# Kernel tuning notes

Hardware: AMD Instinct MI355X
Metric: run time of the kernel (lower is better)

The kernel has to match this reference:

```python
import jax, jax.numpy as jnp
import numpy as np

N_GROUPS = 32
EPS = 1e-5


def group_norm(x, gamma, beta):
    b, c, h, w = x.shape
    xg = x.reshape(b, N_GROUPS, c // N_GROUPS, h, w)
    mean = xg.mean(axis=(2, 3, 4), keepdims=True)
    var = xg.var(axis=(2, 3, 4), keepdims=True)
    xn = ((xg - mean) * jax.lax.rsqrt(var + EPS)).reshape(b, c, h, w)
    return xn * gamma[None, :, None, None] + beta[None, :, None, None]


def conv1x1(x, W, b):
    # x: [b,c,h,w], W: [out,in], b: [out]
    return jnp.einsum('bchw,oc->bohw', x, W) + b[None, :, None, None]


def setup_inputs() -> dict:
    key = jax.random.key(0)
    ks = jax.random.split(key, 6)
    B, C, H, W = 8, 256, 64, 64
    s = 1.0 / np.sqrt(C)
    return {
        'x': jax.random.normal(ks[0], (B, C, H, W), dtype=jnp.float32),
        'norm_gamma': jnp.ones((C,), jnp.float32),
        'norm_beta': jnp.zeros((C,), jnp.float32),
        'Wq': jax.random.normal(ks[1], (C, C), jnp.float32) * s,
        'bq': jnp.zeros((C,), jnp.float32),
        'Wk': jax.random.normal(ks[2], (C, C), jnp.float32) * s,
        'bk': jnp.zeros((C,), jnp.float32),
        'Wv': jax.random.normal(ks[3], (C, C), jnp.float32) * s,
        'bv': jnp.zeros((C,), jnp.float32),
        'Wo': jax.random.normal(ks[4], (C, C), jnp.float32) * s,
        'bo': jnp.zeros((C,), jnp.float32),
    }


def reference(x, norm_gamma, norm_beta, Wq, bq, Wk, bk, Wv, bv, Wo, bo):
    b, c, h, w = x.shape
    hn = group_norm(x, norm_gamma, norm_beta)
    q = conv1x1(hn, Wq, bq).reshape(b, c, h * w)  # [b,c,hw]
    k = conv1x1(hn, Wk, bk).reshape(b, c, h * w)
    v = conv1x1(hn, Wv, bv).reshape(b, c, h * w)
    # scores[b,i,j] = sum_c q[b,c,i] * k[b,c,j]; scale is int(c)*-0.5
    # (faithful to the source, which multiplies by -0.5*c, NOT c**-0.5)
    scores = jnp.einsum('bci,bcj->bij', q, k) * (c * -0.5)
    attn = jax.nn.softmax(scores, axis=2)  # softmax over j (keys)
    # h_[b,c,i] = sum_j v[b,c,j] * attn[b,i,j]
    h_ = jnp.einsum('bcj,bij->bci', v, attn).reshape(b, c, h, w)
    # source applies self.out to the ORIGINAL input x and adds attention output
    return h_ + conv1x1(x, Wo, bo)
```

## Files before the change

kernel.cpp:

```cpp
#include <hip/hip_runtime.h>
#include <hip/hip_bf16.h>


typedef __attribute__((ext_vector_type(8))) short bf16x8;
typedef __attribute__((ext_vector_type(4))) short s16x4;
typedef __attribute__((ext_vector_type(8))) short s16x8;
typedef __attribute__((ext_vector_type(4))) float f32x4;

#define MFMA16(a, b, c) __builtin_amdgcn_mfma_f32_16x16x32_bf16((a), (b), (c), 0, 0, 0)

#define SCALE_Q (-184.66496523378734f)

__device__ __forceinline__ short f2bf(float f) {
  unsigned int u = __builtin_bit_cast(unsigned int, f);
  u = (u + 0x7FFFu + ((u >> 16) & 1u)) >> 16;
  return (short)(unsigned short)u;
}
__device__ __forceinline__ float bf2f(short h) {
  unsigned int u = ((unsigned int)(unsigned short)h) << 16;
  return __builtin_bit_cast(float, u);
}
__device__ __forceinline__ void async16(void* lds, const void* g) {
  __builtin_amdgcn_global_load_lds(
      (const __attribute__((address_space(1))) unsigned int*)g,
      (__attribute__((address_space(3))) unsigned int*)lds, 16, 0, 0);
}

__global__ void wsplit_k(const float* __restrict__ Wq, const float* __restrict__ Wk,
                         const float* __restrict__ Wv, const float* __restrict__ Wo,
                         short* __restrict__ whi, short* __restrict__ wlo) {
  int idx = blockIdx.x * 256 + threadIdx.x;
  int m = idx >> 16;
  int e = idx & 65535;
  const float* W = (m == 0) ? Wq : (m == 1) ? Wk : (m == 2) ? Wv : Wo;
  float v = W[e];
  short h = f2bf(v);
  whi[idx] = h;
  wlo[idx] = f2bf(v - bf2f(h));
}

__global__ void gn_stats_k(const float* __restrict__ x, float* __restrict__ stats) {
  int bg = blockIdx.x;
  int tid = threadIdx.x;
  const float* p = x + (size_t)bg * 32768;
  float s = 0.f, sq = 0.f;
  for (int it = 0; it < 32; ++it) {
    f32x4 v = *(const f32x4*)(p + (size_t)(it * 256 + tid) * 4);
    s += v[0] + v[1] + v[2] + v[3];
    sq += v[0] * v[0] + v[1] * v[1] + v[2] * v[2] + v[3] * v[3];
  }
#pragma unroll
  for (int off = 1; off < 64; off <<= 1) {
    s += __shfl_xor(s, off);
    sq += __shfl_xor(sq, off);
  }
  __shared__ float ls[4], lq[4];
  int w = tid >> 6;
  if ((tid & 63) == 0) { ls[w] = s; lq[w] = sq; }
  __syncthreads();
  if (tid == 0) {
    float S = ls[0] + ls[1] + ls[2] + ls[3];
    float Q = lq[0] + lq[1] + lq[2] + lq[3];
    float mean = S * (1.f / 32768.f);
    float var = Q * (1.f / 32768.f) - mean * mean;
    stats[bg * 2] = mean;
    stats[bg * 2 + 1] = rsqrtf(var + 1e-5f);
  }
}

__global__ void gn_apply_k(const float* __restrict__ x, const float* __restrict__ gamma,
                           const float* __restrict__ beta, const float* __restrict__ stats,
                           short* __restrict__ hn_hi, short* __restrict__ hn_lo) {
  __shared__ float tile[64 * 68];
  int tid = threadIdx.x;
  int b = blockIdx.z, c0 = blockIdx.y * 64, i0 = blockIdx.x * 64;
  int cc = tid >> 4, ich = tid & 15;
#pragma unroll
  for (int it = 0; it < 4; ++it) {
    int c = c0 + cc + it * 16;
    f32x4 vx = *(const f32x4*)(x + ((size_t)(b * 256 + c)) * 4096 + i0 + ich * 4);
    float mean = stats[(b * 32 + (c >> 3)) * 2];
    float rstd = stats[(b * 32 + (c >> 3)) * 2 + 1];
    float ga = gamma[c] * rstd;
    float be = beta[c] - mean * ga;
    f32x4 h = {vx[0] * ga + be, vx[1] * ga + be, vx[2] * ga + be, vx[3] * ga + be};
    *(f32x4*)(&tile[(cc + it * 16) * 68 + ich * 4]) = h;
  }
  __syncthreads();
  int il = tid >> 2, ch = tid & 3;
  s16x8 hv0, hv1, lv0, lv1;
#pragma unroll
  for (int u = 0; u < 16; ++u) {
    float vv = tile[(ch * 16 + u) * 68 + il];
    short h = f2bf(vv);
    short lo = f2bf(vv - bf2f(h));
    if (u < 8) { hv0[u] = h; lv0[u] = lo; } else { hv1[u - 8] = h; lv1[u - 8] = lo; }
  }
  size_t ro = ((size_t)(b * 4096 + i0 + il)) * 256 + c0 + ch * 16;
  *(s16x8*)(hn_hi + ro) = hv0;
  *(s16x8*)(hn_hi + ro + 8) = hv1;
  *(s16x8*)(hn_lo + ro) = lv0;
  *(s16x8*)(hn_lo + ro + 8) = lv1;
}

__global__ __launch_bounds__(256) void proj_qk_k(
    const short* __restrict__ hn_hi, const short* __restrict__ hn_lo,
    const short* __restrict__ whi, const short* __restrict__ wlo,
    const float* __restrict__ bq, const float* __restrict__ bk,
    short* __restrict__ q_hi, short* __restrict__ q_lo,
    short* __restrict__ k_hi, short* __restrict__ k_lo) {
  int tid = threadIdx.x, w = tid >> 6, lane = tid & 63, l4 = lane & 15, g = lane >> 4;
  int iblk = blockIdx.x, y = blockIdx.y, b = blockIdx.z;
  const short* wh = whi + y * 65536;
  const short* wl = wlo + y * 65536;
  const float* bias = y ? bk : bq;
  short* ohi = (y ? k_hi : q_hi) + (size_t)b * 1048576;
  short* olo = (y ? k_lo : q_lo) + (size_t)b * 1048576;
  float scale = y ? 1.0f : SCALE_Q;
  int arow = iblk * 64 + w * 16 + l4;
  const short* ha = hn_hi + ((size_t)(b * 4096 + arow)) * 256 + g * 8;
  const short* la = hn_lo + ((size_t)(b * 4096 + arow)) * 256 + g * 8;
  f32x4 acc[16];
#pragma unroll
  for (int i = 0; i < 16; ++i) acc[i] = (f32x4){0.f, 0.f, 0.f, 0.f};
  for (int ks = 0; ks < 8; ++ks) {
    bf16x8 ah = *(const bf16x8*)(ha + ks * 32);
    bf16x8 al = *(const bf16x8*)(la + ks * 32);
#pragma unroll
    for (int ct = 0; ct < 16; ++ct) {
      bf16x8 bh = *(const bf16x8*)(wh + (ct * 16 + l4) * 256 + ks * 32 + g * 8);
      bf16x8 bl = *(const bf16x8*)(wl + (ct * 16 + l4) * 256 + ks * 32 + g * 8);
      acc[ct] = MFMA16(ah, bh, acc[ct]);
      acc[ct] = MFMA16(al, bh, acc[ct]);
      acc[ct] = MFMA16(ah, bl, acc[ct]);
    }
  }
  int orow = iblk * 64 + w * 16 + g * 4;
#pragma unroll
  for (int ct = 0; ct < 16; ++ct) {
    int c = ct * 16 + l4;
    float bsv = bias[c];
#pragma unroll
    for (int r = 0; r < 4; ++r) {
      float val = (acc[ct][r] + bsv) * scale;
      short h = f2bf(val);
      short lo = f2bf(val - bf2f(h));
      size_t off = ((size_t)(orow + r)) * 256 + c;
      ohi[off] = h;
      olo[off] = lo;
    }
  }
}

__global__ __launch_bounds__(256) void proj_v_k(
    const short* __restrict__ hn_hi, const short* __restrict__ wv_hi,
    const float* __restrict__ bv, short* __restrict__ vout) {
  int tid = threadIdx.x, w = tid >> 6, lane = tid & 63, l4 = lane & 15, g = lane >> 4;
  int jblk = blockIdx.x, cblk = blockIdx.y, b = blockIdx.z;
  int crow = cblk * 64 + w * 16 + l4;
  const short* ap = wv_hi + (size_t)crow * 256 + g * 8;
  f32x4 acc[4];
#pragma unroll
  for (int i = 0; i < 4; ++i) acc[i] = (f32x4){0.f, 0.f, 0.f, 0.f};
  for (int ks = 0; ks < 8; ++ks) {
    bf16x8 a = *(const bf16x8*)(ap + ks * 32);
#pragma unroll
    for (int jt = 0; jt < 4; ++jt) {
      bf16x8 bb = *(const bf16x8*)(hn_hi +
          ((size_t)(b * 4096 + jblk * 64 + jt * 16 + l4)) * 256 + ks * 32 + g * 8);
      acc[jt] = MFMA16(a, bb, acc[jt]);
    }
  }
#pragma unroll
  for (int jt = 0; jt < 4; ++jt) {
#pragma unroll
    for (int r = 0; r < 4; ++r) {
      int c = cblk * 64 + w * 16 + g * 4 + r;
      int j = jblk * 64 + jt * 16 + l4;
      float val = acc[jt][r] + bv[c];
      vout[((size_t)(b * 256 + c)) * 4096 + j] = f2bf(val);
    }
  }
}

__global__ __launch_bounds__(256, 2) void flash3_k(
    const short* __restrict__ qhi, const short* __restrict__ qlo,
    const short* __restrict__ khi, const short* __restrict__ klo,
    const short* __restrict__ vv, const float* __restrict__ x,
    const short* __restrict__ wo_hi, const float* __restrict__ bo,
    float* __restrict__ out) {
  __shared__ short k_hi_s[2][8192];
  __shared__ short k_lo_s[2][8192];
  __shared__ short p_s[2048];
  __shared__ __attribute__((aligned(16))) float albuf[64];
  __shared__ __attribute__((aligned(16))) float flagbuf[4];
  __shared__ __attribute__((aligned(16))) float lsmbuf[64];

  int tid = threadIdx.x, w = tid >> 6, lane = tid & 63, l4 = lane & 15, g = lane >> 4;
  int b = blockIdx.y, i0 = blockIdx.x * 64;
  size_t boff = (size_t)b * 1048576;
  const short* qh_p = qhi + boff;
  const short* ql_p = qlo + boff;
  const char* kh_g = (const char*)(khi + boff);
  const char* kl_g = (const char*)(klo + boff);
  const short* v_p = vv + boff;

  int qrow = i0 + w * 16 + l4;
  bf16x8 qh[8], ql[8];
#pragma unroll
  for (int ks = 0; ks < 8; ++ks) {
    qh[ks] = *(const bf16x8*)(qh_p + (size_t)qrow * 256 + ks * 32 + g * 8);
    ql[ks] = *(const bf16x8*)(ql_p + (size_t)qrow * 256 + ks * 32 + g * 8);
  }

  f32x4 oac[4][4];
#pragma unroll
  for (int it = 0; it < 4; ++it)
#pragma unroll
    for (int ct = 0; ct < 4; ++ct) oac[it][ct] = (f32x4){0.f, 0.f, 0.f, 0.f};
  float m_cur = -1e30f, lsum = 0.f;

  int sx = (l4 & 7) << 4;
  int colx[8];
#pragma unroll
  for (int ks = 0; ks < 8; ++ks) colx[ks] = (ks * 64 + g * 16) ^ sx;
  int krow_b = l4 * 512;

  int ksrc[4];
#pragma unroll
  for (int it = 0; it < 4; ++it) {
    int d = tid * 16 + it * 4096;
    int krow = d >> 9, kcol = d & 511;
    ksrc[it] = krow * 512 + (kcol ^ ((krow & 7) << 4));
  }

  char* khs = (char*)k_hi_s;
  char* kls = (char*)k_lo_s;
  char* ps = (char*)p_s;
  int cbase = w * 64;
  bf16x8 vreg[4];

#pragma unroll
  for (int it = 0; it < 4; ++it) {
    int ldst = w * 1024 + it * 4096;
    async16(khs + ldst, kh_g + ksrc[it]);
    async16(kls + ldst, kl_g + ksrc[it]);
  }

  for (int js = 0; js < 128; ++js) {
    int cur = (js & 1) * 16384;
    __syncthreads();
    if (js < 127) {
      int kgo = (js + 1) * 16384;
      int nxt = ((js + 1) & 1) * 16384;
#pragma unroll
      for (int it = 0; it < 4; ++it) {
        int ldst = nxt + w * 1024 + it * 4096;
        async16(khs + ldst, kh_g + kgo + ksrc[it]);
        async16(kls + ldst, kl_g + kgo + ksrc[it]);
      }
    }
#pragma unroll
    for (int ct = 0; ct < 4; ++ct)
      vreg[ct] = *(const bf16x8*)(v_p + (size_t)(cbase + ct * 16 + l4) * 4096 +
                                  js * 32 + g * 8);

    f32x4 st0 = (f32x4){0.f, 0.f, 0.f, 0.f};
    f32x4 st1 = (f32x4){0.f, 0.f, 0.f, 0.f};
    __builtin_amdgcn_s_setprio(1);
#pragma unroll
    for (int ks = 0; ks < 8; ++ks) {
      bf16x8 kh0 = *(const bf16x8*)(khs + cur + krow_b + colx[ks]);
      bf16x8 kh1 = *(const bf16x8*)(khs + cur + krow_b + colx[ks] + 8192);
      bf16x8 kl0 = *(const bf16x8*)(kls + cur + krow_b + colx[ks]);
      bf16x8 kl1 = *(const bf16x8*)(kls + cur + krow_b + colx[ks] + 8192);
      st0 = MFMA16(kh0, qh[ks], st0);
      st1 = MFMA16(kh1, qh[ks], st1);
      st0 = MFMA16(kl0, qh[ks], st0);
      st1 = MFMA16(kl1, qh[ks], st1);
      st0 = MFMA16(kh0, ql[ks], st0);
      st1 = MFMA16(kh1, ql[ks], st1);
    }
    __builtin_amdgcn_s_setprio(0);

    float pmax = fmaxf(fmaxf(fmaxf(st0[0], st0[1]), fmaxf(st0[2], st0[3])),
                       fmaxf(fmaxf(st1[0], st1[1]), fmaxf(st1[2], st1[3])));
    pmax = fmaxf(pmax, __shfl_xor(pmax, 16));
    pmax = fmaxf(pmax, __shfl_xor(pmax, 32));
    float alpha = 1.0f;
    bool upd = !__all(pmax <= m_cur + 11.0f);
    if (upd) {
      float m_new = fmaxf(m_cur, pmax);
      alpha = exp2f(m_cur - m_new);
      lsum *= alpha;
      m_cur = m_new;
    }
    f32x4 e0, e1;
#pragma unroll
    for (int r = 0; r < 4; ++r) {
      e0[r] = exp2f(st0[r] - m_cur);
      e1[r] = exp2f(st1[r] - m_cur);
    }
    float lps = e0[0] + e0[1] + e0[2] + e0[3] + e1[0] + e1[1] + e1[2] + e1[3];
    lps += __shfl_xor(lps, 16);
    lps += __shfl_xor(lps, 32);
    lsum += lps;

    s16x4 pw0 = {f2bf(e0[0]), f2bf(e0[1]), f2bf(e0[2]), f2bf(e0[3])};
    s16x4 pw1 = {f2bf(e1[0]), f2bf(e1[1]), f2bf(e1[2]), f2bf(e1[3])};
    int wb = (w * 16 + l4) * 64 + g * 8;
    *(s16x4*)(ps + wb) = pw0;
    *(s16x4*)(ps + wb + 32) = pw1;
    if (lane < 16) albuf[w * 16 + lane] = alpha;
    if (lane == 0) flagbuf[w] = upd ? 1.f : 0.f;

    __syncthreads();

    f32x4 fl = *(const f32x4*)(&flagbuf[0]);
    if (fl[0] + fl[1] + fl[2] + fl[3] > 0.f) {
#pragma unroll
      for (int it = 0; it < 4; ++it) {
        f32x4 av = *(const f32x4*)(&albuf[it * 16 + g * 4]);
#pragma unroll
        for (int ct = 0; ct < 4; ++ct)
#pragma unroll
          for (int r = 0; r < 4; ++r) oac[it][ct][r] *= av[r];
      }
    }
#pragma unroll
    for (int it = 0; it < 4; ++it) {
      bf16x8 pf = *(const bf16x8*)(ps + (it * 16 + l4) * 64 + g * 16);
#pragma unroll
      for (int ct = 0; ct < 4; ++ct) oac[it][ct] = MFMA16(pf, vreg[ct], oac[it][ct]);
    }
  }

  if (lane < 16) lsmbuf[w * 16 + lane] = lsum;
  __syncthreads();
#pragma unroll
  for (int it = 0; it < 4; ++it) {
    f32x4 lv = *(const f32x4*)(&lsmbuf[it * 16 + g * 4]);
    f32x4 iv = {1.f / lv[0], 1.f / lv[1], 1.f / lv[2], 1.f / lv[3]};
#pragma unroll
    for (int ct = 0; ct < 4; ++ct)
#pragma unroll
      for (int r = 0; r < 4; ++r) oac[it][ct][r] *= iv[r];
  }
  const float* xb = x + (size_t)b * 1048576;
  for (int ks = 0; ks < 8; ++ks) {
    bf16x8 af[4], bfr[4];
#pragma unroll
    for (int it = 0; it < 4; ++it) {
#pragma unroll
      for (int e = 0; e < 8; ++e) {
        float xv = xb[(size_t)(ks * 32 + g * 8 + e) * 4096 + i0 + it * 16 + l4];
        af[it][e] = f2bf(xv);
      }
    }
#pragma unroll
    for (int ct = 0; ct < 4; ++ct)
      bfr[ct] = *(const bf16x8*)(wo_hi + (cbase + ct * 16 + l4) * 256 + ks * 32 + g * 8);
#pragma unroll
    for (int it = 0; it < 4; ++it)
#pragma unroll
      for (int ct = 0; ct < 4; ++ct) oac[it][ct] = MFMA16(af[it], bfr[ct], oac[it][ct]);
  }
  float* ob = out + (size_t)b * 1048576;
#pragma unroll
  for (int ct = 0; ct < 4; ++ct) {
    float bov = bo[cbase + ct * 16 + l4];
#pragma unroll
    for (int it = 0; it < 4; ++it) {
      float* ad = ob + (size_t)(cbase + ct * 16 + l4) * 4096 + i0 + it * 16 + g * 4;
      f32x4 res;
#pragma unroll
      for (int r = 0; r < 4; ++r) res[r] = oac[it][ct][r] + bov;
      *(f32x4*)ad = res;
    }
  }
}

extern "C" void kernel_launch(void* const* d_in, const int* in_sizes, int n_in,
                              void* d_out, int out_size, void* d_ws, size_t ws_size,
                              hipStream_t stream) {
  (void)in_sizes; (void)n_in; (void)out_size; (void)ws_size;
  const float* x = (const float*)d_in[0];
  const float* gamma = (const float*)d_in[1];
  const float* beta = (const float*)d_in[2];
  const float* Wq = (const float*)d_in[3];
  const float* bq = (const float*)d_in[4];
  const float* Wk = (const float*)d_in[5];
  const float* bk = (const float*)d_in[6];
  const float* Wv = (const float*)d_in[7];
  const float* bv = (const float*)d_in[8];
  const float* Wo = (const float*)d_in[9];
  const float* bo = (const float*)d_in[10];
  float* out = (float*)d_out;
  char* ws = (char*)d_ws;

  const size_t MB16 = 16777216;
  float* stats = (float*)(ws);
  short* whi = (short*)(ws + 4096);
  short* wlo = (short*)(ws + 4096 + 524288);
  char* base = ws + 4096 + 2 * 524288;
  short* hnhi = (short*)(base);
  short* hnlo = (short*)(base + MB16);
  short* qhi = (short*)(base + 2 * MB16);
  short* qlo = (short*)(base + 3 * MB16);
  short* khi = (short*)(base + 4 * MB16);
  short* klo = (short*)(base + 5 * MB16);
  short* vvp = (short*)(base + 6 * MB16);

  wsplit_k<<<dim3(1024), dim3(256), 0, stream>>>(Wq, Wk, Wv, Wo, whi, wlo);
  gn_stats_k<<<dim3(256), dim3(256), 0, stream>>>(x, stats);
  gn_apply_k<<<dim3(64, 4, 8), dim3(256), 0, stream>>>(x, gamma, beta, stats, hnhi, hnlo);
  proj_qk_k<<<dim3(64, 2, 8), dim3(256), 0, stream>>>(hnhi, hnlo, whi, wlo, bq, bk,
                                                      qhi, qlo, khi, klo);
  proj_v_k<<<dim3(64, 4, 8), dim3(256), 0, stream>>>(hnhi, whi + 2 * 65536, bv, vvp);
  flash3_k<<<dim3(64, 8), dim3(256), 0, stream>>>(qhi, qlo, khi, klo, vvp, x,
                                                  whi + 3 * 65536, bo, out);
}
```

Baseline: 537.3 us.

## Enlarge flash attention tile to 128 queries with 8 waves splitting keys

The flash attention kernel now handles 128 query rows per block using 512 threads. Waves are arranged 4x2: each wave owns 32 query rows and half of each 32-key tile. The two halves combine their row max and row sum through LDS exchanges with an added barrier, and the P buffer is padded. Each K tile loaded into LDS now serves twice as many queries, and V register loads are prefetched one iteration ahead. The cost is an extra barrier per iteration, more registers per thread, and half as many blocks (256), which may hurt occupancy on a large GPU.

```diff
diff --git a/kernel.cpp b/kernel.cpp
--- a/kernel.cpp
+++ b/kernel.cpp
@@ -24,6 +24,11 @@
   __builtin_amdgcn_global_load_lds(
       (const __attribute__((address_space(1))) unsigned int*)g,
       (__attribute__((address_space(3))) unsigned int*)lds, 16, 0, 0);
+}
+__device__ __forceinline__ void lgkm_barrier() {
+  asm volatile("s_waitcnt lgkmcnt(0)" ::: "memory");
+  __builtin_amdgcn_s_barrier();
+  __builtin_amdgcn_sched_barrier(0);
 }
 
 __global__ void wsplit_k(const float* __restrict__ Wq, const float* __restrict__ Wk,
@@ -183,7 +188,7 @@
   }
 }
 
-__global__ __launch_bounds__(256, 2) void flash3_k(
+__global__ __launch_bounds__(512, 2) void flash4_k(
     const short* __restrict__ qhi, const short* __restrict__ qlo,
     const short* __restrict__ khi, const short* __restrict__ klo,
     const short* __restrict__ vv, const float* __restrict__ x,
@@ -191,13 +196,15 @@
     float* __restrict__ out) {
   __shared__ short k_hi_s[2][8192];
   __shared__ short k_lo_s[2][8192];
-  __shared__ short p_s[2048];
-  __shared__ __attribute__((aligned(16))) float albuf[64];
+  __shared__ short p_s[128 * 40];
+  __shared__ __attribute__((aligned(16))) float xbuf[2][128];
+  __shared__ __attribute__((aligned(16))) float albuf[128];
+  __shared__ __attribute__((aligned(16))) float lsmbuf[128];
   __shared__ __attribute__((aligned(16))) float flagbuf[4];
-  __shared__ __attribute__((aligned(16))) float lsmbuf[64];
 
   int tid = threadIdx.x, w = tid >> 6, lane = tid & 63, l4 = lane & 15, g = lane >> 4;
-  int b = blockIdx.y, i0 = blockIdx.x * 64;
+  int wj = w & 1, wi = w >> 1;
+  int b = blockIdx.y, i0 = blockIdx.x * 128;
   size_t boff = (size_t)b * 1048576;
   const short* qh_p = qhi + boff;
   const short* ql_p = qlo + boff;
@@ -205,31 +212,35 @@
   const char* kl_g = (const char*)(klo + boff);
   const short* v_p = vv + boff;
 
-  int qrow = i0 + w * 16 + l4;
-  bf16x8 qh[8], ql[8];
-#pragma unroll
-  for (int ks = 0; ks < 8; ++ks) {
-    qh[ks] = *(const bf16x8*)(qh_p + (size_t)qrow * 256 + ks * 32 + g * 8);
-    ql[ks] = *(const bf16x8*)(ql_p + (size_t)qrow * 256 + ks * 32 + g * 8);
-  }
-
-  f32x4 oac[4][4];
-#pragma unroll
-  for (int it = 0; it < 4; ++it)
-#pragma unroll
-    for (int ct = 0; ct < 4; ++ct) oac[it][ct] = (f32x4){0.f, 0.f, 0.f, 0.f};
-  float m_cur = -1e30f, lsum = 0.f;
-
+  bf16x8 qh[2][8], ql[2][8];
+#pragma unroll
+  for (int it = 0; it < 2; ++it) {
+    int qrow = i0 + wi * 32 + it * 16 + l4;
+#pragma unroll
+    for (int ks = 0; ks < 8; ++ks) {
+      qh[it][ks] = *(const bf16x8*)(qh_p + (size_t)qrow * 256 + ks * 32 + g * 8);
+      ql[it][ks] = *(const bf16x8*)(ql_p + (size_t)qrow * 256 + ks * 32 + g * 8);
+    }
+  }
+
+  f32x4 oac[8][2];
+#pragma unroll
+  for (int it = 0; it < 8; ++it) {
+    oac[it][0] = (f32x4){0.f, 0.f, 0.f, 0.f};
+    oac[it][1] = (f32x4){0.f, 0.f, 0.f, 0.f};
+  }
+  float m0 = -1e30f, m1 = -1e30f, ls0 = 0.f, ls1 = 0.f;
+
+  int krow_b = (wj * 16 + l4) * 512;
   int sx = (l4 & 7) << 4;
   int colx[8];
 #pragma unroll
   for (int ks = 0; ks < 8; ++ks) colx[ks] = (ks * 64 + g * 16) ^ sx;
-  int krow_b = l4 * 512;
-
-  int ksrc[4];
-#pragma unroll
-  for (int it = 0; it < 4; ++it) {
-    int d = tid * 16 + it * 4096;
+
+  int ksrc[2];
+#pragma unroll
+  for (int it = 0; it < 2; ++it) {
+    int d = tid * 16 + it * 8192;
     int krow = d >> 9, kcol = d & 511;
     ksrc[it] = krow * 512 + (kcol ^ ((krow & 7) << 4));
   }
@@ -237,15 +248,20 @@
   char* khs = (char*)k_hi_s;
   char* kls = (char*)k_lo_s;
   char* ps = (char*)p_s;
-  int cbase = w * 64;
-  bf16x8 vreg[4];
-
-#pragma unroll
-  for (int it = 0; it < 4; ++it) {
-    int ldst = w * 1024 + it * 4096;
+  int cbase = w * 32;
+  int prow0 = (wi * 32 + l4) * 80 + wj * 32 + g * 8;
+  int prow1 = (wi * 32 + 16 + l4) * 80 + wj * 32 + g * 8;
+
+#pragma unroll
+  for (int it = 0; it < 2; ++it) {
+    int ldst = w * 1024 + it * 8192;
     async16(khs + ldst, kh_g + ksrc[it]);
     async16(kls + ldst, kl_g + ksrc[it]);
   }
+  bf16x8 vreg[2];
+#pragma unroll
+  for (int ct = 0; ct < 2; ++ct)
+    vreg[ct] = *(const bf16x8*)(v_p + (size_t)(cbase + ct * 16 + l4) * 4096 + g * 8);
 
   for (int js = 0; js < 128; ++js) {
     int cur = (js & 1) * 16384;
@@ -254,123 +270,149 @@
       int kgo = (js + 1) * 16384;
       int nxt = ((js + 1) & 1) * 16384;
 #pragma unroll
-      for (int it = 0; it < 4; ++it) {
-        int ldst = nxt + w * 1024 + it * 4096;
+      for (int it = 0; it < 2; ++it) {
+        int ldst = nxt + w * 1024 + it * 8192;
         async16(khs + ldst, kh_g + kgo + ksrc[it]);
         async16(kls + ldst, kl_g + kgo + ksrc[it]);
       }
     }
-#pragma unroll
-    for (int ct = 0; ct < 4; ++ct)
-      vreg[ct] = *(const bf16x8*)(v_p + (size_t)(cbase + ct * 16 + l4) * 4096 +
-                                  js * 32 + g * 8);
-
-    f32x4 st0 = (f32x4){0.f, 0.f, 0.f, 0.f};
-    f32x4 st1 = (f32x4){0.f, 0.f, 0.f, 0.f};
+
+    f32x4 sa0 = (f32x4){0.f, 0.f, 0.f, 0.f};
+    f32x4 sa1 = (f32x4){0.f, 0.f, 0.f, 0.f};
     __builtin_amdgcn_s_setprio(1);
 #pragma unroll
     for (int ks = 0; ks < 8; ++ks) {
-      bf16x8 kh0 = *(const bf16x8*)(khs + cur + krow_b + colx[ks]);
-      bf16x8 kh1 = *(const bf16x8*)(khs + cur + krow_b + colx[ks] + 8192);
-      bf16x8 kl0 = *(const bf16x8*)(kls + cur + krow_b + colx[ks]);
-      bf16x8 kl1 = *(const bf16x8*)(kls + cur + krow_b + colx[ks] + 8192);
-      st0 = MFMA16(kh0, qh[ks], st0);
-      st1 = MFMA16(kh1, qh[ks], st1);
-      st0 = MFMA16(kl0, qh[ks], st0);
-      st1 = MFMA16(kl1, qh[ks], st1);
-      st0 = MFMA16(kh0, ql[ks], st0);
-      st1 = MFMA16(kh1, ql[ks], st1);
+      bf16x8 kh = *(const bf16x8*)(khs + cur + krow_b + colx[ks]);
+      bf16x8 kl = *(const bf16x8*)(kls + cur + krow_b + colx[ks]);
+      sa0 = MFMA16(kh, qh[0][ks], sa0);
+      sa1 = MFMA16(kh, qh[1][ks], sa1);
+      sa0 = MFMA16(kh, ql[0][ks], sa0);
+      sa1 = MFMA16(kh, ql[1][ks], sa1);
+      sa0 = MFMA16(kl, qh[0][ks], sa0);
+      sa1 = MFMA16(kl, qh[1][ks], sa1);
     }
     __builtin_amdgcn_s_setprio(0);
 
-    float pmax = fmaxf(fmaxf(fmaxf(st0[0], st0[1]), fmaxf(st0[2], st0[3])),
-                       fmaxf(fmaxf(st1[0], st1[1]), fmaxf(st1[2], st1[3])));
-    pmax = fmaxf(pmax, __shfl_xor(pmax, 16));
-    pmax = fmaxf(pmax, __shfl_xor(pmax, 32));
-    float alpha = 1.0f;
-    bool upd = !__all(pmax <= m_cur + 11.0f);
+    float pmax0 = fmaxf(fmaxf(sa0[0], sa0[1]), fmaxf(sa0[2], sa0[3]));
+    float pmax1 = fmaxf(fmaxf(sa1[0], sa1[1]), fmaxf(sa1[2], sa1[3]));
+    pmax0 = fmaxf(pmax0, __shfl_xor(pmax0, 16));
+    pmax0 = fmaxf(pmax0, __shfl_xor(pmax0, 32));
+    pmax1 = fmaxf(pmax1, __shfl_xor(pmax1, 16));
+    pmax1 = fmaxf(pmax1, __shfl_xor(pmax1, 32));
+    if (lane < 16) {
+      xbuf[wj][wi * 32 + lane] = pmax0;
+      xbuf[wj][wi * 32 + 16 + lane] = pmax1;
+    }
+    lgkm_barrier();
+
+    pmax0 = fmaxf(pmax0, xbuf[wj ^ 1][wi * 32 + l4]);
+    pmax1 = fmaxf(pmax1, xbuf[wj ^ 1][wi * 32 + 16 + l4]);
+    float alpha0 = 1.0f, alpha1 = 1.0f;
+    bool upd = !__all((pmax0 <= m0 + 11.0f) && (pmax1 <= m1 + 11.0f));
     if (upd) {
-      float m_new = fmaxf(m_cur, pmax);
-      alpha = exp2f(m_cur - m_new);
-      lsum *= alpha;
-      m_cur = m_new;
+      float mn0 = fmaxf(m0, pmax0), mn1 = fmaxf(m1, pmax1);
+      alpha0 = exp2f(m0 - mn0);
+      alpha1 = exp2f(m1 - mn1);
+      ls0 *= alpha0;
+      ls1 *= alpha1;
+      m0 = mn0;
+      m1 = mn1;
     }
     f32x4 e0, e1;
 #pragma unroll
     for (int r = 0; r < 4; ++r) {
-      e0[r] = exp2f(st0[r] - m_cur);
-      e1[r] = exp2f(st1[r] - m_cur);
-    }
-    float lps = e0[0] + e0[1] + e0[2] + e0[3] + e1[0] + e1[1] + e1[2] + e1[3];
-    lps += __shfl_xor(lps, 16);
-    lps += __shfl_xor(lps, 32);
-    lsum += lps;
+      e0[r] = exp2f(sa0[r] - m0);
+      e1[r] = exp2f(sa1[r] - m1);
+    }
+    ls0 += e0[0] + e0[1] + e0[2] + e0[3];
+    ls1 += e1[0] + e1[1] + e1[2] + e1[3];
 
     s16x4 pw0 = {f2bf(e0[0]), f2bf(e0[1]), f2bf(e0[2]), f2bf(e0[3])};
     s16x4 pw1 = {f2bf(e1[0]), f2bf(e1[1]), f2bf(e1[2]), f2bf(e1[3])};
-    int wb = (w * 16 + l4) * 64 + g * 8;
-    *(s16x4*)(ps + wb) = pw0;
-    *(s16x4*)(ps + wb + 32) = pw1;
-    if (lane < 16) albuf[w * 16 + lane] = alpha;
-    if (lane == 0) flagbuf[w] = upd ? 1.f : 0.f;
-
-    __syncthreads();
+    *(s16x4*)(ps + prow0) = pw0;
+    *(s16x4*)(ps + prow1) = pw1;
+    if (wj == 0 && lane < 16) {
+      albuf[wi * 32 + lane] = alpha0;
+      albuf[wi * 32 + 16 + lane] = alpha1;
+    }
+    if (wj == 0 && lane == 0) flagbuf[wi] = upd ? 1.f : 0.f;
+    lgkm_barrier();
 
     f32x4 fl = *(const f32x4*)(&flagbuf[0]);
     if (fl[0] + fl[1] + fl[2] + fl[3] > 0.f) {
 #pragma unroll
-      for (int it = 0; it < 4; ++it) {
+      for (int it = 0; it < 8; ++it) {
         f32x4 av = *(const f32x4*)(&albuf[it * 16 + g * 4]);
 #pragma unroll
-        for (int ct = 0; ct < 4; ++ct)
-#pragma unroll
-          for (int r = 0; r < 4; ++r) oac[it][ct][r] *= av[r];
+        for (int r = 0; r < 4; ++r) {
+          oac[it][0][r] *= av[r];
+          oac[it][1][r] *= av[r];
+        }
       }
     }
 #pragma unroll
-    for (int it = 0; it < 4; ++it) {
-      bf16x8 pf = *(const bf16x8*)(ps + (it * 16 + l4) * 64 + g * 16);
-#pragma unroll
-      for (int ct = 0; ct < 4; ++ct) oac[it][ct] = MFMA16(pf, vreg[ct], oac[it][ct]);
-    }
-  }
-
-  if (lane < 16) lsmbuf[w * 16 + lane] = lsum;
-  __syncthreads();
-#pragma unroll
-  for (int it = 0; it < 4; ++it) {
-    f32x4 lv = *(const f32x4*)(&lsmbuf[it * 16 + g * 4]);
-    f32x4 iv = {1.f / lv[0], 1.f / lv[1], 1.f / lv[2], 1.f / lv[3]};
-#pragma unroll
-    for (int ct = 0; ct < 4; ++ct)
-#pragma unroll
-      for (int r = 0; r < 4; ++r) oac[it][ct][r] *= iv[r];
+    for (int it = 0; it < 8; ++it) {
+      bf16x8 pf = *(const bf16x8*)(ps + (it * 16 + l4) * 80 + g * 16);
+      oac[it][0] = MFMA16(pf, vreg[0], oac[it][0]);
+      oac[it][1] = MFMA16(pf, vreg[1], oac[it][1]);
+    }
+    if (js < 127) {
+#pragma unroll
+      for (int ct = 0; ct < 2; ++ct)
+        vreg[ct] = *(const bf16x8*)(v_p + (size_t)(cbase + ct * 16 + l4) * 4096 +
+                                    (js + 1) * 32 + g * 8);
+    }
+  }
+
+  ls0 += __shfl_xor(ls0, 16);
+  ls0 += __shfl_xor(ls0, 32);
+  ls1 += __shfl_xor(ls1, 16);
+  ls1 += __shfl_xor(ls1, 32);
+  if (lane < 16) {
+    xbuf[wj][wi * 32 + lane] = ls0;
+    xbuf[wj][wi * 32 + 16 + lane] = ls1;
+  }
+  lgkm_barrier();
+  float t0 = ls0 + xbuf[wj ^ 1][wi * 32 + l4];
+  float t1 = ls1 + xbuf[wj ^ 1][wi * 32 + 16 + l4];
+  if (wj == 0 && lane < 16) {
+    lsmbuf[wi * 32 + l4] = 1.f / t0;
+    lsmbuf[wi * 32 + 16 + l4] = 1.f / t1;
+  }
+  lgkm_barrier();
+#pragma unroll
+  for (int it = 0; it < 8; ++it) {
+    f32x4 iv = *(const f32x4*)(&lsmbuf[it * 16 + g * 4]);
+#pragma unroll
+    for (int r = 0; r < 4; ++r) {
+      oac[it][0][r] *= iv[r];
+      oac[it][1][r] *= iv[r];
+    }
   }
   const float* xb = x + (size_t)b * 1048576;
   for (int ks = 0; ks < 8; ++ks) {
-    bf16x8 af[4], bfr[4];
-#pragma unroll
-    for (int it = 0; it < 4; ++it) {
+    bf16x8 bfr[2];
+#pragma unroll
+    for (int ct = 0; ct < 2; ++ct)
+      bfr[ct] = *(const bf16x8*)(wo_hi + (cbase + ct * 16 + l4) * 256 + ks * 32 + g * 8);
+#pragma unroll
+    for (int it = 0; it < 8; ++it) {
+      bf16x8 af;
 #pragma unroll
       for (int e = 0; e < 8; ++e) {
         float xv = xb[(size_t)(ks * 32 + g * 8 + e) * 4096 + i0 + it * 16 + l4];
-        af[it][e] = f2bf(xv);
+        af[e] = f2bf(xv);
       }
-    }
-#pragma unroll
-    for (int ct = 0; ct < 4; ++ct)
-      bfr[ct] = *(const bf16x8*)(wo_hi + (cbase + ct * 16 + l4) * 256 + ks * 32 + g * 8);
-#pragma unroll
-    for (int it = 0; it < 4; ++it)
-#pragma unroll
-      for (int ct = 0; ct < 4; ++ct) oac[it][ct] = MFMA16(af[it], bfr[ct], oac[it][ct]);
+      oac[it][0] = MFMA16(af, bfr[0], oac[it][0]);
+      oac[it][1] = MFMA16(af, bfr[1], oac[it][1]);
+    }
   }
   float* ob = out + (size_t)b * 1048576;
 #pragma unroll
-  for (int ct = 0; ct < 4; ++ct) {
+  for (int ct = 0; ct < 2; ++ct) {
     float bov = bo[cbase + ct * 16 + l4];
 #pragma unroll
-    for (int it = 0; it < 4; ++it) {
+    for (int it = 0; it < 8; ++it) {
       float* ad = ob + (size_t)(cbase + ct * 16 + l4) * 4096 + i0 + it * 16 + g * 4;
       f32x4 res;
 #pragma unroll
@@ -417,6 +459,6 @@
   proj_qk_k<<<dim3(64, 2, 8), dim3(256), 0, stream>>>(hnhi, hnlo, whi, wlo, bq, bk,
                                                       qhi, qlo, khi, klo);
   proj_v_k<<<dim3(64, 4, 8), dim3(256), 0, stream>>>(hnhi, whi + 2 * 65536, bv, vvp);
-  flash3_k<<<dim3(64, 8), dim3(256), 0, stream>>>(qhi, qlo, khi, klo, vvp, x,
+  flash4_k<<<dim3(32, 8), dim3(512), 0, stream>>>(qhi, qlo, khi, klo, vvp, x,
                                                   whi + 3 * 65536, bo, out);
 }
```

Result: slower. 653.6 us (+21.6%).

## Rewrite flash attention kernel with 32x32 MFMA tiles and 64-key steps

Applied to the files above, without the earlier changes.

The attention kernel now uses 32x32x16 bf16 MFMA instead of 16x16x32. Work is split across a 2x2 wave grid (query halves by key halves), and each iteration processes 64 keys instead of 32. The K tile is single-buffered with a vmcnt barrier, and its next load is issued after the score phase. Row maxima and sums are exchanged across waves through LDS, with lighter custom barriers. The aim is higher MFMA throughput and fewer loop iterations and barriers, at the cost of losing double-buffer overlap on K loads and adding cross-wave reductions.

```diff
diff --git a/kernel.cpp b/kernel.cpp
--- a/kernel.cpp
+++ b/kernel.cpp
@@ -6,8 +6,10 @@
 typedef __attribute__((ext_vector_type(4))) short s16x4;
 typedef __attribute__((ext_vector_type(8))) short s16x8;
 typedef __attribute__((ext_vector_type(4))) float f32x4;
+typedef __attribute__((ext_vector_type(16))) float f32x16;
 
 #define MFMA16(a, b, c) __builtin_amdgcn_mfma_f32_16x16x32_bf16((a), (b), (c), 0, 0, 0)
+#define MFMA32(a, b, c) __builtin_amdgcn_mfma_f32_32x32x16_bf16((a), (b), (c), 0, 0, 0)
 
 #define SCALE_Q (-184.66496523378734f)
 
@@ -24,6 +26,16 @@
   __builtin_amdgcn_global_load_lds(
       (const __attribute__((address_space(1))) unsigned int*)g,
       (__attribute__((address_space(3))) unsigned int*)lds, 16, 0, 0);
+}
+__device__ __forceinline__ void lgkm_barrier() {
+  asm volatile("s_waitcnt lgkmcnt(0)" ::: "memory");
+  __builtin_amdgcn_s_barrier();
+  __builtin_amdgcn_sched_barrier(0);
+}
+__device__ __forceinline__ void vm_barrier() {
+  asm volatile("s_waitcnt vmcnt(0)" ::: "memory");
+  __builtin_amdgcn_s_barrier();
+  __builtin_amdgcn_sched_barrier(0);
 }
 
 __global__ void wsplit_k(const float* __restrict__ Wq, const float* __restrict__ Wk,
@@ -183,20 +195,23 @@
   }
 }
 
-__global__ __launch_bounds__(256, 2) void flash3_k(
+__global__ __launch_bounds__(256, 2) void flash5_k(
     const short* __restrict__ qhi, const short* __restrict__ qlo,
     const short* __restrict__ khi, const short* __restrict__ klo,
     const short* __restrict__ vv, const float* __restrict__ x,
     const short* __restrict__ wo_hi, const float* __restrict__ bo,
     float* __restrict__ out) {
-  __shared__ short k_hi_s[2][8192];
-  __shared__ short k_lo_s[2][8192];
-  __shared__ short p_s[2048];
+  __shared__ short k_hi_s[16384];
+  __shared__ short k_lo_s[16384];
+  __shared__ short p_s[4096];
+  __shared__ __attribute__((aligned(16))) float xbuf[2][64];
   __shared__ __attribute__((aligned(16))) float albuf[64];
-  __shared__ __attribute__((aligned(16))) float flagbuf[4];
   __shared__ __attribute__((aligned(16))) float lsmbuf[64];
-
-  int tid = threadIdx.x, w = tid >> 6, lane = tid & 63, l4 = lane & 15, g = lane >> 4;
+  __shared__ __attribute__((aligned(16))) float flagbuf[2];
+
+  int tid = threadIdx.x, w = tid >> 6, lane = tid & 63;
+  int l31 = lane & 31, hi = lane >> 5;
+  int wj = w & 1, wi = w >> 1;
   int b = blockIdx.y, i0 = blockIdx.x * 64;
   size_t boff = (size_t)b * 1048576;
   const short* qh_p = qhi + boff;
@@ -204,179 +219,184 @@
   const char* kh_g = (const char*)(khi + boff);
   const char* kl_g = (const char*)(klo + boff);
   const short* v_p = vv + boff;
-
-  int qrow = i0 + w * 16 + l4;
-  bf16x8 qh[8], ql[8];
-#pragma unroll
-  for (int ks = 0; ks < 8; ++ks) {
-    qh[ks] = *(const bf16x8*)(qh_p + (size_t)qrow * 256 + ks * 32 + g * 8);
-    ql[ks] = *(const bf16x8*)(ql_p + (size_t)qrow * 256 + ks * 32 + g * 8);
-  }
-
-  f32x4 oac[4][4];
-#pragma unroll
-  for (int it = 0; it < 4; ++it)
-#pragma unroll
-    for (int ct = 0; ct < 4; ++ct) oac[it][ct] = (f32x4){0.f, 0.f, 0.f, 0.f};
+  int cbase = w * 64;
+
+  int qrow = i0 + wi * 32 + l31;
+  bf16x8 qh[16], ql[16];
+#pragma unroll
+  for (int ks = 0; ks < 16; ++ks) {
+    qh[ks] = *(const bf16x8*)(qh_p + (size_t)qrow * 256 + ks * 16 + hi * 8);
+    ql[ks] = *(const bf16x8*)(ql_p + (size_t)qrow * 256 + ks * 16 + hi * 8);
+  }
+
+  f32x16 oac[2][2];
+#pragma unroll
+  for (int ih = 0; ih < 2; ++ih) {
+    oac[ih][0] = (f32x16)0.0f;
+    oac[ih][1] = (f32x16)0.0f;
+  }
   float m_cur = -1e30f, lsum = 0.f;
-
-  int sx = (l4 & 7) << 4;
-  int colx[8];
-#pragma unroll
-  for (int ks = 0; ks < 8; ++ks) colx[ks] = (ks * 64 + g * 16) ^ sx;
-  int krow_b = l4 * 512;
-
-  int ksrc[4];
-#pragma unroll
-  for (int it = 0; it < 4; ++it) {
-    int d = tid * 16 + it * 4096;
-    int krow = d >> 9, kcol = d & 511;
-    ksrc[it] = krow * 512 + (kcol ^ ((krow & 7) << 4));
-  }
 
   char* khs = (char*)k_hi_s;
   char* kls = (char*)k_lo_s;
   char* ps = (char*)p_s;
-  int cbase = w * 64;
-  bf16x8 vreg[4];
-
-#pragma unroll
-  for (int it = 0; it < 4; ++it) {
-    int ldst = w * 1024 + it * 4096;
-    async16(khs + ldst, kh_g + ksrc[it]);
-    async16(kls + ldst, kl_g + ksrc[it]);
-  }
-
-  for (int js = 0; js < 128; ++js) {
-    int cur = (js & 1) * 16384;
-    __syncthreads();
-    if (js < 127) {
-      int kgo = (js + 1) * 16384;
-      int nxt = ((js + 1) & 1) * 16384;
-#pragma unroll
-      for (int it = 0; it < 4; ++it) {
-        int ldst = nxt + w * 1024 + it * 4096;
-        async16(khs + ldst, kh_g + kgo + ksrc[it]);
-        async16(kls + ldst, kl_g + kgo + ksrc[it]);
+  int krb = (wj * 32 + l31) * 512;
+  int psw = (l31 & 7) << 4;
+  int ksl[16];
+#pragma unroll
+  for (int ks = 0; ks < 16; ++ks) ksl[ks] = (ks * 32 + hi * 16) ^ psw;
+
+  int soff[8];
+#pragma unroll
+  for (int it = 0; it < 8; ++it) {
+    int row = w * 16 + it * 2 + hi;
+    soff[it] = row * 512 + ((l31 * 16) ^ ((row & 7) << 4));
+  }
+
+#pragma unroll
+  for (int it = 0; it < 8; ++it) {
+    async16(khs + w * 8192 + it * 1024, kh_g + soff[it]);
+    async16(kls + w * 8192 + it * 1024, kl_g + soff[it]);
+  }
+
+  int pwb = (wi * 32 + l31) * 128;
+
+  for (int js = 0; js < 64; ++js) {
+    vm_barrier();
+
+    f32x16 sacc = (f32x16)0.0f;
+    __builtin_amdgcn_s_setprio(1);
+#pragma unroll
+    for (int ks = 0; ks < 16; ++ks) {
+      bf16x8 kh = *(const bf16x8*)(khs + krb + ksl[ks]);
+      bf16x8 kl = *(const bf16x8*)(kls + krb + ksl[ks]);
+      sacc = MFMA32(kh, qh[ks], sacc);
+      sacc = MFMA32(kl, qh[ks], sacc);
+      sacc = MFMA32(kh, ql[ks], sacc);
+    }
+    __builtin_amdgcn_s_setprio(0);
+
+    float pm = sacc[0];
+#pragma unroll
+    for (int t = 1; t < 16; ++t) pm = fmaxf(pm, sacc[t]);
+    pm = fmaxf(pm, __shfl_xor(pm, 32));
+    if (lane < 32) xbuf[wj][wi * 32 + l31] = pm;
+    lgkm_barrier();
+
+    bf16x8 vf[2][4];
+#pragma unroll
+    for (int ct = 0; ct < 2; ++ct)
+#pragma unroll
+      for (int j4 = 0; j4 < 4; ++j4)
+        vf[ct][j4] = *(const bf16x8*)(v_p + (size_t)(cbase + ct * 32 + l31) * 4096 +
+                                      js * 64 + j4 * 16 + hi * 8);
+    if (js < 63) {
+      int tb = (js + 1) * 32768;
+#pragma unroll
+      for (int it = 0; it < 8; ++it) {
+        async16(khs + w * 8192 + it * 1024, kh_g + tb + soff[it]);
+        async16(kls + w * 8192 + it * 1024, kl_g + tb + soff[it]);
       }
     }
-#pragma unroll
-    for (int ct = 0; ct < 4; ++ct)
-      vreg[ct] = *(const bf16x8*)(v_p + (size_t)(cbase + ct * 16 + l4) * 4096 +
-                                  js * 32 + g * 8);
-
-    f32x4 st0 = (f32x4){0.f, 0.f, 0.f, 0.f};
-    f32x4 st1 = (f32x4){0.f, 0.f, 0.f, 0.f};
-    __builtin_amdgcn_s_setprio(1);
-#pragma unroll
-    for (int ks = 0; ks < 8; ++ks) {
-      bf16x8 kh0 = *(const bf16x8*)(khs + cur + krow_b + colx[ks]);
-      bf16x8 kh1 = *(const bf16x8*)(khs + cur + krow_b + colx[ks] + 8192);
-      bf16x8 kl0 = *(const bf16x8*)(kls + cur + krow_b + colx[ks]);
-      bf16x8 kl1 = *(const bf16x8*)(kls + cur + krow_b + colx[ks] + 8192);
-      st0 = MFMA16(kh0, qh[ks], st0);
-      st1 = MFMA16(kh1, qh[ks], st1);
-      st0 = MFMA16(kl0, qh[ks], st0);
-      st1 = MFMA16(kl1, qh[ks], st1);
-      st0 = MFMA16(kh0, ql[ks], st0);
-      st1 = MFMA16(kh1, ql[ks], st1);
-    }
-    __builtin_amdgcn_s_setprio(0);
-
-    float pmax = fmaxf(fmaxf(fmaxf(st0[0], st0[1]), fmaxf(st0[2], st0[3])),
-                       fmaxf(fmaxf(st1[0], st1[1]), fmaxf(st1[2], st1[3])));
-    pmax = fmaxf(pmax, __shfl_xor(pmax, 16));
-    pmax = fmaxf(pmax, __shfl_xor(pmax, 32));
+
+    pm = fmaxf(pm, xbuf[wj ^ 1][wi * 32 + l31]);
     float alpha = 1.0f;
-    bool upd = !__all(pmax <= m_cur + 11.0f);
+    bool upd = !__all(pm <= m_cur + 11.0f);
     if (upd) {
-      float m_new = fmaxf(m_cur, pmax);
-      alpha = exp2f(m_cur - m_new);
+      float mn = fmaxf(m_cur, pm);
+      alpha = exp2f(m_cur - mn);
       lsum *= alpha;
-      m_cur = m_new;
-    }
-    f32x4 e0, e1;
-#pragma unroll
-    for (int r = 0; r < 4; ++r) {
-      e0[r] = exp2f(st0[r] - m_cur);
-      e1[r] = exp2f(st1[r] - m_cur);
-    }
-    float lps = e0[0] + e0[1] + e0[2] + e0[3] + e1[0] + e1[1] + e1[2] + e1[3];
-    lps += __shfl_xor(lps, 16);
+      m_cur = mn;
+    }
+    float e[16];
+    float lps = 0.f;
+#pragma unroll
+    for (int t = 0; t < 16; ++t) {
+      e[t] = exp2f(sacc[t] - m_cur);
+      lps += e[t];
+    }
     lps += __shfl_xor(lps, 32);
     lsum += lps;
 
-    s16x4 pw0 = {f2bf(e0[0]), f2bf(e0[1]), f2bf(e0[2]), f2bf(e0[3])};
-    s16x4 pw1 = {f2bf(e1[0]), f2bf(e1[1]), f2bf(e1[2]), f2bf(e1[3])};
-    int wb = (w * 16 + l4) * 64 + g * 8;
-    *(s16x4*)(ps + wb) = pw0;
-    *(s16x4*)(ps + wb + 32) = pw1;
-    if (lane < 16) albuf[w * 16 + lane] = alpha;
-    if (lane == 0) flagbuf[w] = upd ? 1.f : 0.f;
-
-    __syncthreads();
-
-    f32x4 fl = *(const f32x4*)(&flagbuf[0]);
-    if (fl[0] + fl[1] + fl[2] + fl[3] > 0.f) {
-#pragma unroll
-      for (int it = 0; it < 4; ++it) {
-        f32x4 av = *(const f32x4*)(&albuf[it * 16 + g * 4]);
-#pragma unroll
-        for (int ct = 0; ct < 4; ++ct)
-#pragma unroll
-          for (int r = 0; r < 4; ++r) oac[it][ct][r] *= av[r];
+#pragma unroll
+    for (int qq = 0; qq < 4; ++qq) {
+      s16x4 pw = {f2bf(e[qq * 4]), f2bf(e[qq * 4 + 1]),
+                  f2bf(e[qq * 4 + 2]), f2bf(e[qq * 4 + 3])};
+      *(s16x4*)(ps + pwb + ((wj * 64 + qq * 16 + hi * 8) ^ psw)) = pw;
+    }
+    if (wj == 0 && lane < 32) albuf[wi * 32 + l31] = alpha;
+    if (wj == 0 && lane == 0) flagbuf[wi] = upd ? 1.f : 0.f;
+    lgkm_barrier();
+
+    if (flagbuf[0] + flagbuf[1] > 0.f) {
+#pragma unroll
+      for (int ih = 0; ih < 2; ++ih)
+#pragma unroll
+        for (int qq = 0; qq < 4; ++qq) {
+          f32x4 av = *(const f32x4*)(&albuf[ih * 32 + qq * 8 + hi * 4]);
+#pragma unroll
+          for (int t = 0; t < 4; ++t) {
+            oac[ih][0][qq * 4 + t] *= av[t];
+            oac[ih][1][qq * 4 + t] *= av[t];
+          }
+        }
+    }
+#pragma unroll
+    for (int ih = 0; ih < 2; ++ih)
+#pragma unroll
+      for (int j4 = 0; j4 < 4; ++j4) {
+        bf16x8 pf = *(const bf16x8*)(ps + (ih * 32 + l31) * 128 +
+                                     ((j4 * 32 + hi * 16) ^ psw));
+        oac[ih][0] = MFMA32(pf, vf[0][j4], oac[ih][0]);
+        oac[ih][1] = MFMA32(pf, vf[1][j4], oac[ih][1]);
       }
-    }
-#pragma unroll
-    for (int it = 0; it < 4; ++it) {
-      bf16x8 pf = *(const bf16x8*)(ps + (it * 16 + l4) * 64 + g * 16);
-#pragma unroll
-      for (int ct = 0; ct < 4; ++ct) oac[it][ct] = MFMA16(pf, vreg[ct], oac[it][ct]);
-    }
-  }
-
-  if (lane < 16) lsmbuf[w * 16 + lane] = lsum;
-  __syncthreads();
-#pragma unroll
-  for (int it = 0; it < 4; ++it) {
-    f32x4 lv = *(const f32x4*)(&lsmbuf[it * 16 + g * 4]);
-    f32x4 iv = {1.f / lv[0], 1.f / lv[1], 1.f / lv[2], 1.f / lv[3]};
-#pragma unroll
-    for (int ct = 0; ct < 4; ++ct)
-#pragma unroll
-      for (int r = 0; r < 4; ++r) oac[it][ct][r] *= iv[r];
-  }
+  }
+
+  if (lane < 32) xbuf[wj][wi * 32 + l31] = lsum;
+  lgkm_barrier();
+  float ltot = lsum + xbuf[wj ^ 1][wi * 32 + l31];
+  if (wj == 0 && lane < 32) lsmbuf[wi * 32 + l31] = 1.f / ltot;
+  lgkm_barrier();
+#pragma unroll
+  for (int ih = 0; ih < 2; ++ih)
+#pragma unroll
+    for (int qq = 0; qq < 4; ++qq) {
+      f32x4 iv = *(const f32x4*)(&lsmbuf[ih * 32 + qq * 8 + hi * 4]);
+#pragma unroll
+      for (int t = 0; t < 4; ++t) {
+        oac[ih][0][qq * 4 + t] *= iv[t];
+        oac[ih][1][qq * 4 + t] *= iv[t];
+      }
+    }
   const float* xb = x + (size_t)b * 1048576;
-  for (int ks = 0; ks < 8; ++ks) {
-    bf16x8 af[4], bfr[4];
-#pragma unroll
-    for (int it = 0; it < 4; ++it) {
-#pragma unroll
-      for (int e = 0; e < 8; ++e) {
-        float xv = xb[(size_t)(ks * 32 + g * 8 + e) * 4096 + i0 + it * 16 + l4];
-        af[it][e] = f2bf(xv);
+  for (int ks = 0; ks < 16; ++ks) {
+    bf16x8 bfr0 = *(const bf16x8*)(wo_hi + (cbase + l31) * 256 + ks * 16 + hi * 8);
+    bf16x8 bfr1 = *(const bf16x8*)(wo_hi + (cbase + 32 + l31) * 256 + ks * 16 + hi * 8);
+#pragma unroll
+    for (int ih = 0; ih < 2; ++ih) {
+      bf16x8 af;
+#pragma unroll
+      for (int e2 = 0; e2 < 8; ++e2) {
+        float xv = xb[(size_t)(ks * 16 + hi * 8 + e2) * 4096 + i0 + ih * 32 + l31];
+        af[e2] = f2bf(xv);
       }
-    }
-#pragma unroll
-    for (int ct = 0; ct < 4; ++ct)
-      bfr[ct] = *(const bf16x8*)(wo_hi + (cbase + ct * 16 + l4) * 256 + ks * 32 + g * 8);
-#pragma unroll
-    for (int it = 0; it < 4; ++it)
-#pragma unroll
-      for (int ct = 0; ct < 4; ++ct) oac[it][ct] = MFMA16(af[it], bfr[ct], oac[it][ct]);
+      oac[ih][0] = MFMA32(af, bfr0, oac[ih][0]);
+      oac[ih][1] = MFMA32(af, bfr1, oac[ih][1]);
+    }
   }
   float* ob = out + (size_t)b * 1048576;
 #pragma unroll
-  for (int ct = 0; ct < 4; ++ct) {
-    float bov = bo[cbase + ct * 16 + l4];
-#pragma unroll
-    for (int it = 0; it < 4; ++it) {
-      float* ad = ob + (size_t)(cbase + ct * 16 + l4) * 4096 + i0 + it * 16 + g * 4;
-      f32x4 res;
-#pragma unroll
-      for (int r = 0; r < 4; ++r) res[r] = oac[it][ct][r] + bov;
-      *(f32x4*)ad = res;
-    }
+  for (int ct = 0; ct < 2; ++ct) {
+    float bov = bo[cbase + ct * 32 + l31];
+    float* cb = ob + (size_t)(cbase + ct * 32 + l31) * 4096 + i0;
+#pragma unroll
+    for (int ih = 0; ih < 2; ++ih)
+#pragma unroll
+      for (int qq = 0; qq < 4; ++qq) {
+        f32x4 res = {oac[ih][ct][qq * 4] + bov, oac[ih][ct][qq * 4 + 1] + bov,
+                     oac[ih][ct][qq * 4 + 2] + bov, oac[ih][ct][qq * 4 + 3] + bov};
+        *(f32x4*)(cb + ih * 32 + qq * 8 + hi * 4) = res;
+      }
   }
 }
 
@@ -417,6 +437,6 @@
   proj_qk_k<<<dim3(64, 2, 8), dim3(256), 0, stream>>>(hnhi, hnlo, whi, wlo, bq, bk,
                                                       qhi, qlo, khi, klo);
   proj_v_k<<<dim3(64, 4, 8), dim3(256), 0, stream>>>(hnhi, whi + 2 * 65536, bv, vvp);
-  flash3_k<<<dim3(64, 8), dim3(256), 0, stream>>>(qhi, qlo, khi, klo, vvp, x,
+  flash5_k<<<dim3(64, 8), dim3(256), 0, stream>>>(qhi, qlo, khi, klo, vvp, x,
                                                   whi + 3 * 65536, bo, out);
 }
```

Result: slower. 1.035 ms (+92.6%).
